# Kernel tuning notes

Hardware: AMD Instinct MI355X
Metric: run time of the kernel (lower is better)

## Reference

```python
import jax, jax.numpy as jnp
import numpy as np

A = 3                      # anchors per location
HS = [256, 128, 64, 32]    # square feature-map sizes (FPN levels)
B = 4                      # batch (num images)
SIZES = [A * h * h for h in HS]
T = sum(SIZES)             # 261120 anchors per image
PRE_N, POST_N = 512, 512
NMS_TH, SCORE_TH, MIN_SIZE = 0.7, 0.0, 1e-3
LOG_MAX = 4.135166556742356   # log(1000/16), standard delta clamp
MAXV = 8                      # max vertices of quad-quad intersection
LVL_OFF = 8192.0              # per-level coordinate offset for batched NMS


def box_corners(b):
    # b: [..., 5] (cx, cy, w, h, angle) -> [..., 4, 2] CCW corners
    cx, cy, w, h, a = (b[..., i] for i in range(5))
    c, s = jnp.cos(a), jnp.sin(a)
    dx = 0.5 * jnp.stack([w, -w, -w, w], -1)
    dy = 0.5 * jnp.stack([h, h, -h, -h], -1)
    x = cx[..., None] + dx * c[..., None] - dy * s[..., None]
    y = cy[..., None] + dx * s[..., None] + dy * c[..., None]
    return jnp.stack([x, y], -1)


def _clip(poly, cnt, p1, p2):
    # Sutherland-Hodgman clip of poly (padded [MAXV,2], cnt valid) by half-plane left of p1->p2
    e = p2 - p1
    d = e[0] * (poly[:, 1] - p1[1]) - e[1] * (poly[:, 0] - p1[0])
    def body(carry, i):
        out, oc = carry
        nxt = jnp.where(i + 1 < cnt, i + 1, 0)
        cur_in, nxt_in = d[i] >= 0, d[nxt] >= 0
        valid = i < cnt
        keep = valid & cur_in
        out = out.at[oc].set(jnp.where(keep, poly[i], out[oc]))
        oc = oc + keep.astype(jnp.int32)
        crs = valid & (cur_in != nxt_in)
        den = d[i] - d[nxt]
        t = d[i] / jnp.where(den == 0, 1.0, den)
        ip = poly[i] + t * (poly[nxt] - poly[i])
        out = out.at[oc].set(jnp.where(crs, ip, out[oc]))
        oc = oc + crs.astype(jnp.int32)
        return (out, oc), None
    (out, oc), _ = jax.lax.scan(body, (jnp.zeros((MAXV, 2), poly.dtype), jnp.int32(0)), jnp.arange(MAXV))
    return out, oc


def _inter_area(ca, cb):
    # intersection area of two convex quads given CCW corners [4,2]
    poly = jnp.zeros((MAXV, 2), ca.dtype).at[:4].set(ca)
    cnt = jnp.int32(4)
    for k in range(4):
        poly, cnt = _clip(poly, cnt, cb[k], cb[(k + 1) % 4])
    i = jnp.arange(MAXV)
    nxt = jnp.where(i + 1 < cnt, i + 1, 0)
    cr = poly[i, 0] * poly[nxt, 1] - poly[nxt, 0] * poly[i, 1]
    area = 0.5 * jnp.abs(jnp.sum(jnp.where(i < cnt, cr, 0.0)))
    return jnp.where(cnt >= 3, area, 0.0)


def decode(deltas, anchors):
    # XYWHA decode with 6-dim deltas (dx,dy,dw,dh,dsin,dcos), weights all 1.0
    ax, ay, aw, ah, aa = (anchors[..., i] for i in range(5))
    dx, dy, dw, dh, ds, dc = (deltas[..., i] for i in range(6))
    dw = jnp.minimum(dw, LOG_MAX)
    dh = jnp.minimum(dh, LOG_MAX)
    return jnp.stack([ax + dx * aw, ay + dy * ah, aw * jnp.exp(dw),
                      ah * jnp.exp(dh), aa + jnp.arctan2(ds, dc)], -1)


def nms_image(boxes, scores, levels):
    # boxes [N,5], scores [N] (post-sigmoid), levels [N] int32 -> fixed-size padded outputs
    N = scores.shape[0]
    valid = (boxes[:, 2] >= MIN_SIZE) & (boxes[:, 3] >= MIN_SIZE) & (scores >= SCORE_TH)
    s = jnp.where(valid, scores, -jnp.inf)
    order = jnp.argsort(-s)
    bx, sc, vd = boxes[order], s[order], valid[order]
    off = levels[order].astype(bx.dtype) * LVL_OFF
    nb = bx.at[:, :2].add(off[:, None])          # level offset => cross-level IoU == 0
    nbg = jax.lax.stop_gradient(nb)
    corners = box_corners(nbg)                    # [N,4,2]
    areas = nbg[:, 2] * nbg[:, 3]
    CH = 128
    def chunk_fn(args):
        cc, ca = args
        def row(ci, ai):
            inter = jax.vmap(lambda cj: _inter_area(ci, cj))(corners)
            return inter / (ai + areas - inter + 1e-7)
        return jax.vmap(row)(cc, ca)
    iou = jax.lax.map(chunk_fn, (corners.reshape(N // CH, CH, 4, 2),
                                 areas.reshape(N // CH, CH))).reshape(N, N)
    idx = jnp.arange(N)
    def body(i, sup):
        keep_i = ~sup[i]
        return sup | (keep_i & (iou[i] > NMS_TH) & (idx > i))
    sup = jax.lax.fori_loop(0, N, body, ~vd)      # invalid boxes start suppressed
    kept = ~sup
    _, top_i = jax.lax.top_k(jnp.where(kept, sc, -jnp.inf), POST_N)
    ok = kept[top_i]
    return jnp.where(ok[:, None], bx[top_i], 0.0), jnp.where(ok, sc[top_i], 0.0)


def rpn_forward(objs, dlts, anchors):
    obj_f, dlt_f = [], []
    for o, d, h in zip(objs, dlts, HS):
        # permute_and_flatten: [B,A,H,W] -> [B,H*W*A]; [B,A*6,H,W] -> [B,H*W*A,6]
        obj_f.append(o.transpose(0, 2, 3, 1).reshape(B, -1))
        dlt_f.append(d.reshape(B, A, 6, h, h).transpose(0, 3, 4, 1, 2).reshape(B, -1, 6))
    objectness = jnp.concatenate(obj_f, 1)        # [B, T]
    deltas = jnp.concatenate(dlt_f, 1)            # [B, T, 6]
    proposals = decode(deltas, anchors)           # [B, T, 5]
    parts, offset = [], 0
    for sz in SIZES:                               # per-level top-k
        k = min(PRE_N, sz)
        _, ti = jax.lax.top_k(objectness[:, offset:offset + sz], k)
        parts.append(ti + offset)
        offset += sz
    top_idx = jnp.concatenate(parts, 1)           # [B, 4*PRE_N]
    levels = jnp.concatenate([jnp.full((sz,), i, jnp.int32) for i, sz in enumerate(SIZES)])
    obj_top = jnp.take_along_axis(objectness, top_idx, 1)
    prop_top = jnp.take_along_axis(proposals, top_idx[..., None], 1)
    lvl_top = levels[top_idx]
    scores = jax.nn.sigmoid(obj_top)
    return jax.vmap(nms_image)(prop_top, scores, lvl_top)


def setup_inputs() -> dict:
    key = jax.random.key(0)
    ks = jax.random.split(key, 9)
    inp = {}
    for i, h in enumerate(HS):
        inp[f"obj{i}"] = jax.random.normal(ks[i], (B, A, h, h), jnp.float32)
        inp[f"dlt{i}"] = 0.25 * jax.random.normal(ks[4 + i], (B, A * 6, h, h), jnp.float32)
    u = jax.random.uniform(ks[8], (B, T, 5), jnp.float32)
    inp["anchors"] = jnp.stack([u[..., 0] * 1024.0, u[..., 1] * 1024.0,
                                8.0 + 120.0 * u[..., 2], 8.0 + 120.0 * u[..., 3],
                                jnp.pi * (u[..., 4] - 0.5)], -1)
    return inp


def reference(obj0, obj1, obj2, obj3, dlt0, dlt1, dlt2, dlt3, anchors):
    # returns (boxes [B, POST_N, 5], scores [B, POST_N]) padded with zeros
    return rpn_forward([obj0, obj1, obj2, obj3], [dlt0, dlt1, dlt2, dlt3], anchors)
```

## Files before the change

### kernel.cpp

```cpp
#include <hip/hip_runtime.h>

typedef unsigned int u32;
typedef unsigned long long u64;
typedef unsigned char u8;

#define NB 4
#define T_ANCH 261120
#define NCAND 2048
#define KSEL 512
#define POSTN 512
#define LOG_MAXF 4.135166556742356f
#define NMS_TH 0.7f
#define LVL_OFF_F 8192.0f
#define BINS 4096
#define EQCAP 8192
#define K4A_BLOCKS 2048
#define K4A_ROWS 4
#define K1_BLOCKS 256

__device__ __forceinline__ u32 mono32(float f){
  u32 u = __float_as_uint(f);
  return (u & 0x80000000u) ? ~u : (u | 0x80000000u);
}
__device__ __forceinline__ int lvl_hw(int lvl){ return 65536 >> (2*lvl); }
__device__ __forceinline__ int lvl_off(int lvl){
  return (lvl>0?196608:0) + (lvl>1?49152:0) + (lvl>2?12288:0);
}
__device__ __forceinline__ void k1_map(int bx, int& b, int& lvl, int& ch){
  b = bx >> 6;
  int c = bx & 63;
  if (c < 48){ lvl = 0; ch = c; }
  else if (c < 60){ lvl = 1; ch = c - 48; }
  else if (c < 63){ lvl = 2; ch = c - 60; }
  else { lvl = 3; ch = 0; }
}

__global__ __launch_bounds__(1024) void k1_hist_thresh(
    const float* __restrict__ o0, const float* __restrict__ o1,
    const float* __restrict__ o2, const float* __restrict__ o3,
    u32* __restrict__ hist16, u32* __restrict__ done16,
    u32* __restrict__ gb0, u32* __restrict__ gcA)
{
  int b, lvl, ch;
  k1_map(blockIdx.x, b, lvl, ch);
  int bid16 = b*4 + lvl;
  int nch = (lvl==0?48 : lvl==1?12 : lvl==2?3 : 1);
  const float* ob = (lvl==0)?o0 : (lvl==1)?o1 : (lvl==2)?o2 : o3;
  int hw = lvl_hw(lvl);
  int size = 3*hw;
  int n4 = size >> 2;
  int i4 = ch*1024 + threadIdx.x;
  __shared__ u32 hist[BINS];
  __shared__ u32 coarse[64];
  __shared__ int s_last;
  for (int i = threadIdx.x; i < BINS; i += 1024) hist[i] = 0;
  __syncthreads();
  if (i4 < n4){
    float4 v = ((const float4*)(ob + (size_t)b*size))[i4];
    atomicAdd(&hist[mono32(v.x) >> 20], 1u);
    atomicAdd(&hist[mono32(v.y) >> 20], 1u);
    atomicAdd(&hist[mono32(v.z) >> 20], 1u);
    atomicAdd(&hist[mono32(v.w) >> 20], 1u);
  }
  __syncthreads();
  u32* gh = hist16 + (size_t)bid16*BINS;
  for (int i = threadIdx.x; i < BINS; i += 1024){
    u32 c = hist[i];
    if (c) atomicAdd(&gh[i], c);
  }
  __syncthreads();
  if (threadIdx.x == 0){
    __threadfence();
    u32 d = atomicAdd(&done16[bid16], 1u);
    s_last = (d == (u32)(nch - 1)) ? 1 : 0;
  }
  __syncthreads();
  if (!s_last) return;

  __threadfence();
  for (int i = threadIdx.x; i < BINS; i += 1024)
    hist[i] = __hip_atomic_load(&gh[i], __ATOMIC_RELAXED, __HIP_MEMORY_SCOPE_AGENT);
  __syncthreads();
  int t = threadIdx.x;
  if (t < 64){
    u32 s = 0;
    for (int z = 0; z < 64; ++z) s += hist[t*64 + z];
    coarse[t] = s;
  }
  __syncthreads();
  if (t == 0){
    u32 acc = 0;
    int cb = 63;
    while (acc + coarse[cb] < (u32)KSEL){ acc += coarse[cb]; --cb; }
    int z = cb*64 + 63;
    while (acc + hist[z] < (u32)KSEL){ acc += hist[z]; --z; }
    gb0[bid16] = (u32)z;
    gcA[bid16] = acc;
  }
}

__global__ __launch_bounds__(1024) void k2_classify(
    const float* __restrict__ o0, const float* __restrict__ o1,
    const float* __restrict__ o2, const float* __restrict__ o3,
    const u32* __restrict__ gb0,
    u32* __restrict__ emitcnt, u32* __restrict__ tiecnt,
    int* __restrict__ cand_j, u64* __restrict__ gtie)
{
  int b, lvl, ch;
  k1_map(blockIdx.x, b, lvl, ch);
  int bid16 = b*4 + lvl;
  const float* ob = (lvl==0)?o0 : (lvl==1)?o1 : (lvl==2)?o2 : o3;
  int hw = lvl_hw(lvl);
  int size = 3*hw;
  int n4 = size >> 2;
  int i4 = ch*1024 + threadIdx.x;

  __shared__ u32 dbuf[KSEL];
  __shared__ u64 tbuf[4096];
  __shared__ u32 dn, tn, dbase, tbase;
  if (threadIdx.x == 0){ dn = 0; tn = 0; }
  __syncthreads();

  u32 b0v = gb0[bid16];
  if (i4 < n4){
    float4 v = ((const float4*)(ob + (size_t)b*size))[i4];
    int L = i4 << 2;
    int a = L / hw;
    int pix = L - a*hw;
    int j0 = pix*3 + a;
    float vv[4] = {v.x, v.y, v.z, v.w};
    #pragma unroll
    for (int q = 0; q < 4; ++q){
      u32 m = mono32(vv[q]);
      u32 bin = m >> 20;
      int j = j0 + 3*q;
      if (bin > b0v){
        u32 s = atomicAdd(&dn, 1u);
        if (s < (u32)KSEL) dbuf[s] = (u32)j;
      } else if (bin == b0v){
        u32 s = atomicAdd(&tn, 1u);
        if (s < 4096u) tbuf[s] = ((u64)m << 32) | (u32)(~(u32)j);
      }
    }
  }
  __syncthreads();
  if (threadIdx.x == 0){
    dbase = dn ? atomicAdd(&emitcnt[bid16], dn) : 0u;
    tbase = tn ? atomicAdd(&tiecnt[bid16], tn) : 0u;
  }
  __syncthreads();
  for (u32 x = threadIdx.x; x < dn; x += 1024){
    u32 s = dbase + x;
    if (s < (u32)KSEL) cand_j[bid16*KSEL + s] = (int)dbuf[x];
  }
  for (u32 x = threadIdx.x; x < tn; x += 1024){
    u32 s = tbase + x;
    if (s < (u32)EQCAP) gtie[(size_t)bid16*EQCAP + s] = tbuf[x];
  }
}

__global__ __launch_bounds__(512) void k3_tie_decode(
    const u64* __restrict__ gtie, const u32* __restrict__ tiecnt,
    const u32* __restrict__ gcA, const int* __restrict__ cand_j,
    const float* __restrict__ o0, const float* __restrict__ o1,
    const float* __restrict__ o2, const float* __restrict__ o3,
    const float* __restrict__ d0, const float* __restrict__ d1,
    const float* __restrict__ d2, const float* __restrict__ d3,
    const float* __restrict__ anchors,
    float* __restrict__ cscore, u32* __restrict__ csmono,
    u64* __restrict__ ctb, float* __restrict__ cbox, u8* __restrict__ cvalid)
{
  int bid = blockIdx.x;
  int t = threadIdx.x;
  __shared__ u64 eq[EQCAP];
  __shared__ u32 wbuf[KSEL];
  __shared__ int jlist[KSEL];
  __shared__ u32 wn;
  u32 n = tiecnt[bid]; if (n > (u32)EQCAP) n = (u32)EQCAP;
  u32 cA = gcA[bid];
  u32 k = (u32)KSEL - cA;
  if (t == 0) wn = 0;
  for (int i = t; i < KSEL; i += 512) jlist[i] = 0;
  for (u32 i = t; i < n; i += 512) eq[i] = gtie[(size_t)bid*EQCAP + i];
  __syncthreads();
  for (u32 i = t; i < n; i += 512){
    u64 ki = eq[i];
    u32 r = 0;
    for (u32 m = 0; m < n; ++m) r += (eq[m] > ki) ? 1u : 0u;
    if (r < k){
      u32 s = atomicAdd(&wn, 1u);
      if (s < (u32)KSEL) wbuf[s] = (u32)(~(u32)ki);
    }
  }
  __syncthreads();
  u32 w = wn;
  for (u32 i = t; i < cA; i += 512)
    if (i < (u32)KSEL) jlist[i] = cand_j[bid*KSEL + i];
  for (u32 x = t; x < w; x += 512){
    u32 s = cA + x;
    if (s < (u32)KSEL) jlist[s] = (int)wbuf[x];
  }
  __syncthreads();

  {
    int c = bid*KSEL + t;
    int b = bid >> 2, lvl = bid & 3;
    int j = jlist[t];
    int hw = lvl_hw(lvl);
    u32 pix = (u32)j / 3u;
    u32 a = (u32)j - pix*3u;
    const float* ob = (lvl==0)?o0 : (lvl==1)?o1 : (lvl==2)?o2 : o3;
    const float* dl = (lvl==0)?d0 : (lvl==1)?d1 : (lvl==2)?d2 : d3;

    float ov = ob[(size_t)(b*3 + (int)a)*hw + pix];
    size_t dbase = ((size_t)(b*3 + (int)a)*6)*(size_t)hw + pix;
    float dx  = dl[dbase + 0*(size_t)hw];
    float dy  = dl[dbase + 1*(size_t)hw];
    float dw  = dl[dbase + 2*(size_t)hw];
    float dh  = dl[dbase + 3*(size_t)hw];
    float dsn = dl[dbase + 4*(size_t)hw];
    float dcs = dl[dbase + 5*(size_t)hw];
    int tt = lvl_off(lvl) + j;
    const float* an = anchors + ((size_t)b*T_ANCH + tt)*5;
    float ax=an[0], ay=an[1], aw=an[2], ah=an[3], aa=an[4];
    dw = fminf(dw, LOG_MAXF); dh = fminf(dh, LOG_MAXF);
    float cx = ax + dx*aw;
    float cy = ay + dy*ah;
    float ww = aw * expf(dw);
    float hh = ah * expf(dh);
    float ang = aa + atan2f(dsn, dcs);
    double sd = 1.0 / (1.0 + exp(-(double)ov));
    float sc = (float)sd;
    bool valid = (ww >= 1e-3f) && (hh >= 1e-3f) && (sc >= 0.0f);
    cscore[c] = sc;
    csmono[c] = valid ? mono32(sc) : 0u;
    ctb[c] = ((u64)lvl << 50) | ((u64)(u32)(~mono32(ov)) << 18) | (u64)(u32)j;
    cvalid[c] = valid ? 1 : 0;
    float* bb = cbox + (size_t)c*5;
    bb[0]=cx; bb[1]=cy; bb[2]=ww; bb[3]=hh; bb[4]=ang;
  }
}

__global__ __launch_bounds__(256) void k4_rank(
    const u32* __restrict__ csmono, const u64* __restrict__ ctb,
    const float* __restrict__ cscore, const float* __restrict__ cbox,
    const u8* __restrict__ cvalid,
    float* __restrict__ sscore, float* __restrict__ sbox,
    float* __restrict__ geom, float4* __restrict__ aabb4,
    u8* __restrict__ svalid)
{
  int b   = blockIdx.x >> 6;
  int blk = blockIdx.x & 63;
  __shared__ u32 sm[NCAND];
  __shared__ u64 stb[NCAND];
  __shared__ u32 cnt[32][8];
  for (int k = threadIdx.x; k < NCAND; k += 256){
    sm[k]  = csmono[b*NCAND + k];
    stb[k] = ctb[b*NCAND + k];
  }
  __syncthreads();
  int esub = threadIdx.x >> 3;
  int ssub = threadIdx.x & 7;
  int id = blk*32 + esub;
  u32 ms = sm[id];
  u64 mt = stb[id];
  u32 r = 0;
  #pragma unroll 8
  for (int it = 0; it < 256; ++it){
    int m = it*8 + ssub;
    u32 s2 = sm[m]; u64 t2 = stb[m];
    r += ((s2 > ms) || (s2 == ms && t2 < mt)) ? 1u : 0u;
  }
  cnt[esub][ssub] = r;
  __syncthreads();
  if (ssub == 0){
    u32 rank = 0;
    #pragma unroll
    for (int q = 0; q < 8; ++q) rank += cnt[esub][q];
    int gsrc = b*NCAND + id;
    int gdst = b*NCAND + (int)rank;
    sscore[gdst] = cscore[gsrc];
    svalid[gdst] = cvalid[gsrc];
    float b0 = cbox[(size_t)gsrc*5+0], b1 = cbox[(size_t)gsrc*5+1];
    float b2 = cbox[(size_t)gsrc*5+2], b3 = cbox[(size_t)gsrc*5+3];
    float b4 = cbox[(size_t)gsrc*5+4];
    float* sb = sbox + (size_t)gdst*5;
    sb[0]=b0; sb[1]=b1; sb[2]=b2; sb[3]=b3; sb[4]=b4;
    int lvl = (int)((mt >> 50) & 3ull);
    float offv = (float)lvl * LVL_OFF_F;
    float cx = b0 + offv, cy = b1 + offv, w=b2, h=b3, ang=b4;
    float cc = cosf(ang), sn = sinf(ang);
    float hx = 0.5f*w, hy = 0.5f*h;
    float x0 = cx + hx*cc - hy*sn, y0 = cy + hx*sn + hy*cc;
    float x1 = cx - hx*cc - hy*sn, y1 = cy - hx*sn + hy*cc;
    float x2 = cx - hx*cc + hy*sn, y2 = cy - hx*sn - hy*cc;
    float x3 = cx + hx*cc + hy*sn, y3 = cy + hx*sn - hy*cc;
    float minx = fminf(fminf(x0,x1),fminf(x2,x3));
    float maxx = fmaxf(fmaxf(x0,x1),fmaxf(x2,x3));
    float miny = fminf(fminf(y0,y1),fminf(y2,y3));
    float maxy = fmaxf(fmaxf(y0,y1),fmaxf(y2,y3));
    float* g = geom + (size_t)gdst*16;
    g[0]=minx; g[1]=maxx; g[2]=miny; g[3]=maxy; g[4]=w*h;
    g[5]=x0; g[6]=y0; g[7]=x1; g[8]=y1; g[9]=x2; g[10]=y2; g[11]=x3; g[12]=y3;
    aabb4[gdst] = make_float4(minx, maxx, miny, maxy);
  }
}

__device__ __forceinline__ void emit_pt(float* ox, float* oy, int oc, float x, float y){
  #pragma unroll
  for (int s = 0; s < 8; ++s) if (s == oc){ ox[s] = x; oy[s] = y; }
}

__device__ float quad_inter(const float* ca, const float* cb){
  float px[8], py[8];
  #pragma unroll
  for (int q = 0; q < 8; ++q){ px[q]=0.f; py[q]=0.f; }
  #pragma unroll
  for (int q = 0; q < 4; ++q){ px[q]=ca[2*q]; py[q]=ca[2*q+1]; }
  int cnt = 4;
  #pragma unroll
  for (int e = 0; e < 4; ++e){
    float p1x = cb[2*e],         p1y = cb[2*e+1];
    float p2x = cb[(2*e+2)&7],   p2y = cb[(2*e+3)&7];
    float ex = p2x-p1x, ey = p2y-p1y;
    float d[8];
    #pragma unroll
    for (int q = 0; q < 8; ++q) d[q] = ex*(py[q]-p1y) - ey*(px[q]-p1x);
    float ox[8], oy[8];
    #pragma unroll
    for (int q = 0; q < 8; ++q){ ox[q]=0.f; oy[q]=0.f; }
    int oc = 0;
    #pragma unroll
    for (int q = 0; q < 8; ++q){
      if (q < cnt){
        bool last = (q+1 >= cnt);
        float dn  = last ? d[0]  : d[(q+1)&7];
        bool in0 = (d[q] >= 0.0f), in1 = (dn >= 0.0f);
        if (in0){ emit_pt(ox,oy,oc,px[q],py[q]); oc++; }
        if (in0 != in1){
          float pnx = last ? px[0] : px[(q+1)&7];
          float pny = last ? py[0] : py[(q+1)&7];
          float den = d[q] - dn;
          float t = d[q] / ((den == 0.0f) ? 1.0f : den);
          emit_pt(ox,oy,oc, px[q] + t*(pnx-px[q]), py[q] + t*(pny-py[q]));
          oc++;
        }
      }
    }
    cnt = (oc > 8) ? 8 : oc;
    #pragma unroll
    for (int q = 0; q < 8; ++q){ px[q]=ox[q]; py[q]=oy[q]; }
  }
  if (cnt < 3) return 0.0f;
  float s = 0.0f;
  #pragma unroll
  for (int q = 0; q < 8; ++q){
    if (q < cnt){
      bool last = (q+1 >= cnt);
      float pnx = last ? px[0] : px[(q+1)&7];
      float pny = last ? py[0] : py[(q+1)&7];
      s += px[q]*pny - pnx*py[q];
    }
  }
  return 0.5f*fabsf(s);
}

__global__ __launch_bounds__(256) void k5_pairs(
    const float4* __restrict__ aabb4, const float* __restrict__ geom,
    u64* __restrict__ mask, u64* __restrict__ rowflag)
{
  __shared__ u32 lbuf[K4A_ROWS*NCAND];
  __shared__ u32 lcnt;
  if (threadIdx.x == 0) lcnt = 0;
  __syncthreads();
  int img = blockIdx.x >> 9;
  int i0  = (blockIdx.x & 511) * K4A_ROWS;
  #pragma unroll
  for (int r = 0; r < K4A_ROWS; ++r){
    int i = i0 + r;
    float4 gi = aabb4[img*NCAND + i];
    for (int j = threadIdx.x; j < NCAND; j += 256){
      bool pass = false;
      if (j > i){
        float4 gj = aabb4[img*NCAND + j];
        pass = !(gi.x > gj.y || gj.x > gi.y || gi.z > gj.w || gj.z > gi.w);
      }
      if (pass){
        u32 s = atomicAdd(&lcnt, 1u);
        lbuf[s] = (u32)((i << 11) | j);
      }
    }
  }
  __syncthreads();
  u32 n = lcnt;
  for (u32 x = threadIdx.x; x < n; x += 256){
    u32 gt = lbuf[x];
    int i = (int)(gt >> 11);
    int j = (int)(gt & (NCAND-1));
    const float* gi = geom + ((size_t)(img*NCAND + i))*16;
    const float* gj = geom + ((size_t)(img*NCAND + j))*16;
    float inter = quad_inter(gi+5, gj+5);
    float iou = inter / (gi[4] + gj[4] - inter + 1e-7f);
    if (iou > NMS_TH){
      atomicOr(&mask[((size_t)(img*NCAND + i))*32 + (j >> 6)], 1ull << (j & 63));
      atomicOr(&rowflag[(size_t)img*32 + (i >> 6)], 1ull << (i & 63));
    }
  }
}

__global__ __launch_bounds__(1024) void k6_nms_out(
    const u64* __restrict__ mask, const u64* __restrict__ rowflag,
    const u8* __restrict__ svalid,
    const float* __restrict__ sbox, const float* __restrict__ sscore,
    float* __restrict__ out)
{
  int b = blockIdx.x;
  __shared__ u32 fid[NCAND];
  __shared__ u32 wcnt[32], wpref[32];
  __shared__ u64 s_kept[32];
  __shared__ u32 pref[32];
  __shared__ u32 s_F;
  int t = threadIdx.x;
  int wid = t >> 6, lane = t & 63;

  if (t < 32) wcnt[t] = (u32)__popcll(rowflag[b*32 + t]);
  __syncthreads();
  if (t == 0){
    u32 run = 0;
    for (int w = 0; w < 32; ++w){ wpref[w] = run; run += wcnt[w]; }
    s_F = run;
  }
  __syncthreads();
  if (t < 32){
    u64 fw = rowflag[b*32 + t];
    u32 o = wpref[t];
    while (fw){
      int bpos = __builtin_ctzll(fw);
      fid[o++] = (u32)(t*64 + bpos);
      fw &= fw - 1;
    }
  }
  for (int x = t; x < POSTN*5; x += 1024) out[(size_t)b*POSTN*5 + x] = 0.0f;
  for (int x = t; x < POSTN;   x += 1024) out[(size_t)NB*POSTN*5 + b*POSTN + x] = 0.0f;
  __syncthreads();

  if (wid == 0){
    u32 slo = 0, shi = 0;
    {
      int wl = lane & 31;
      u64 w = 0;
      for (int q = 0; q < 64; ++q)
        if (!svalid[b*NCAND + wl*64 + q]) w |= (1ull << q);
      slo = (u32)w; shi = (u32)(w >> 32);
    }
    u32 F = s_F;
    const u64* mb = mask + ((size_t)b*NCAND)*32;
    for (u32 f = 0; f < F; f += 8){
      u32 myfid = 0;
      if (f + (lane & 7) < F) myfid = fid[f + (lane & 7)];
      u64 v[8];
      #pragma unroll
      for (int q = 0; q < 8; ++q){
        if (f + q < F){
          u32 fq = (u32)__builtin_amdgcn_readlane((int)myfid, q);
          v[q] = mb[(size_t)fq*32 + (lane & 31)];
        } else v[q] = 0ull;
      }
      #pragma unroll
      for (int q = 0; q < 8; ++q){
        if (f + q < F){
          u32 i = (u32)__builtin_amdgcn_readlane((int)myfid, q);
          int wi = (int)(i >> 6);
          u32 wlo = (u32)__builtin_amdgcn_readlane((int)slo, wi);
          u32 whi = (u32)__builtin_amdgcn_readlane((int)shi, wi);
          u64 w = ((u64)whi << 32) | wlo;
          u32 keep = (u32)((~w >> (i & 63)) & 1ull);
          u64 vm = v[q] & (0ull - (u64)keep);
          slo |= (u32)vm; shi |= (u32)(vm >> 32);
        }
      }
    }
    if (lane < 32) s_kept[lane] = ~(((u64)shi << 32) | slo);
  }
  __syncthreads();

  if (t < 32) pref[t] = (u32)__popcll(s_kept[t]);
  __syncthreads();
  if (t == 0){
    u32 run = 0;
    for (int w = 0; w < 32; ++w){ u32 tv = pref[w]; pref[w] = run; run += tv; }
  }
  __syncthreads();
  for (int i = t; i < NCAND; i += 1024){
    u64 kw = s_kept[i >> 6];
    if ((kw >> (i & 63)) & 1ull){
      u32 rank = pref[i >> 6] + (u32)__popcll(kw & ((1ull << (i & 63)) - 1ull));
      if (rank < POSTN){
        const float* bp = sbox + ((size_t)(b*NCAND + i))*5;
        float* op = out + ((size_t)(b*POSTN + rank))*5;
        op[0]=bp[0]; op[1]=bp[1]; op[2]=bp[2]; op[3]=bp[3]; op[4]=bp[4];
        out[(size_t)NB*POSTN*5 + b*POSTN + rank] = sscore[b*NCAND + i];
      }
    }
  }
}

extern "C" void kernel_launch(void* const* d_in, const int* in_sizes, int n_in,
                              void* d_out, int out_size, void* d_ws, size_t ws_size,
                              hipStream_t stream)
{
  (void)out_size; (void)ws_size;
  const float *obj[4] = {nullptr,nullptr,nullptr,nullptr};
  const float *dlt[4] = {nullptr,nullptr,nullptr,nullptr};
  const float *anchors = nullptr;
  for (int i = 0; i < n_in; ++i){
    int s = in_sizes[i];
    const float* p = (const float*)d_in[i];
    switch (s){
      case 786432:  obj[0] = p; break;
      case 4718592: dlt[0] = p; break;
      case 196608:  obj[1] = p; break;
      case 1179648: dlt[1] = p; break;
      case 49152:   obj[2] = p; break;
      case 294912:  dlt[2] = p; break;
      case 12288:   obj[3] = p; break;
      case 73728:   dlt[3] = p; break;
      case 5222400: anchors = p; break;
      default: break;
    }
  }

  char* wsb = (char*)d_ws;
  size_t off = 0;
  auto alloc = [&](size_t bytes)->void*{
    size_t cur = (off + 255) & ~(size_t)255;
    off = cur + bytes;
    return (void*)(wsb + cur);
  };
  int*   cand_j = (int*)  alloc(16*KSEL*sizeof(int));
  float* cscore = (float*)alloc((size_t)NB*NCAND*sizeof(float));
  u32*   csmono = (u32*)  alloc((size_t)NB*NCAND*sizeof(u32));
  u64*   ctb    = (u64*)  alloc((size_t)NB*NCAND*sizeof(u64));
  float* cbox   = (float*)alloc((size_t)NB*NCAND*5*sizeof(float));
  u8*    cvalid = (u8*)   alloc((size_t)NB*NCAND);
  float* sscore = (float*)alloc((size_t)NB*NCAND*sizeof(float));
  float* sbox   = (float*)alloc((size_t)NB*NCAND*5*sizeof(float));
  u8*    svalid = (u8*)   alloc((size_t)NB*NCAND);
  float* geom   = (float*)alloc((size_t)NB*NCAND*16*sizeof(float));
  float4* aabb4 = (float4*)alloc((size_t)NB*NCAND*sizeof(float4));
  u64*   gtie   = (u64*)  alloc((size_t)16*EQCAP*sizeof(u64));
  u32*   gb0    = (u32*)  alloc(16*sizeof(u32));
  u32*   gcA    = (u32*)  alloc(16*sizeof(u32));
  size_t mask_bytes = (size_t)NB*NCAND*32*sizeof(u64);
  u64*   maskp  = (u64*)  alloc(mask_bytes);
  u64*   rowflag= (u64*)  alloc((size_t)NB*32*sizeof(u64));
  u32*   hist16 = (u32*)  alloc((size_t)16*BINS*sizeof(u32));
  u32*   done16 = (u32*)  alloc(16*sizeof(u32));
  u32*   emitc  = (u32*)  alloc(16*sizeof(u32));
  u32*   tiec   = (u32*)  alloc(16*sizeof(u32));
  size_t zero_len = (size_t)((wsb + off) - (char*)maskp);

  hipMemsetAsync(maskp, 0, zero_len, stream);

  hipLaunchKernelGGL(k1_hist_thresh, dim3(K1_BLOCKS), dim3(1024), 0, stream,
                     obj[0], obj[1], obj[2], obj[3], hist16, done16, gb0, gcA);
  hipLaunchKernelGGL(k2_classify, dim3(K1_BLOCKS), dim3(1024), 0, stream,
                     obj[0], obj[1], obj[2], obj[3], gb0, emitc, tiec,
                     cand_j, gtie);
  hipLaunchKernelGGL(k3_tie_decode, dim3(16), dim3(512), 0, stream,
                     gtie, tiec, gcA, cand_j,
                     obj[0], obj[1], obj[2], obj[3],
                     dlt[0], dlt[1], dlt[2], dlt[3],
                     anchors, cscore, csmono, ctb, cbox, cvalid);
  hipLaunchKernelGGL(k4_rank, dim3(256), dim3(256), 0, stream,
                     csmono, ctb, cscore, cbox, cvalid, sscore, sbox, geom,
                     aabb4, svalid);
  hipLaunchKernelGGL(k5_pairs, dim3(K4A_BLOCKS), dim3(256), 0, stream,
                     aabb4, geom, maskp, rowflag);
  hipLaunchKernelGGL(k6_nms_out, dim3(4), dim3(1024), 0, stream,
                     maskp, rowflag, svalid, sbox, sscore, (float*)d_out);
}
```

Baseline: 204.6 us.

## Balance NMS pair rows, ballot-aggregate atomics, move mask zeroing into rank kernel

The pair-test kernel now gives each block two low rows and two mirrored high rows, so the triangular j>i work per block is roughly equal. The inner loop starts at i+1, and wave-level ballot plus a single atomicAdd per wave compacts the passing pairs, replacing one shared atomic per pair. The 2 MB mask and rowflag zeroing moves out of the memset and into the rank kernel, so the memset covers only the small counters. The local buffer shrinks to 4096 entries, which still holds the worst case for the balanced rows (about 4096 pairs).

New measurement: 192.3 us. 6.0% less time.

```diff
diff --git a/kernel.cpp b/kernel.cpp
--- a/kernel.cpp
+++ b/kernel.cpp
@@ -14,8 +14,7 @@
 #define LVL_OFF_F 8192.0f
 #define BINS 4096
 #define EQCAP 8192
-#define K4A_BLOCKS 2048
-#define K4A_ROWS 4
+#define K5_BLOCKS 2048
 #define K1_BLOCKS 256
 
 __device__ __forceinline__ u32 mono32(float f){
@@ -247,13 +246,18 @@
     const u8* __restrict__ cvalid,
     float* __restrict__ sscore, float* __restrict__ sbox,
     float* __restrict__ geom, float4* __restrict__ aabb4,
-    u8* __restrict__ svalid)
+    u8* __restrict__ svalid, u64* __restrict__ maskz, u64* __restrict__ rowflagz)
 {
   int b   = blockIdx.x >> 6;
   int blk = blockIdx.x & 63;
   __shared__ u32 sm[NCAND];
   __shared__ u64 stb[NCAND];
   __shared__ u32 cnt[32][8];
+  {
+    u64* mz = maskz + (size_t)blockIdx.x * 1024;
+    for (int x = threadIdx.x; x < 1024; x += 256) mz[x] = 0ull;
+    if (threadIdx.x == 0 && blockIdx.x < NB*32) rowflagz[blockIdx.x] = 0ull;
+  }
   for (int k = threadIdx.x; k < NCAND; k += 256){
     sm[k]  = csmono[b*NCAND + k];
     stb[k] = ctb[b*NCAND + k];
@@ -369,25 +373,31 @@
     const float4* __restrict__ aabb4, const float* __restrict__ geom,
     u64* __restrict__ mask, u64* __restrict__ rowflag)
 {
-  __shared__ u32 lbuf[K4A_ROWS*NCAND];
+  __shared__ u32 lbuf[4096];
   __shared__ u32 lcnt;
   if (threadIdx.x == 0) lcnt = 0;
   __syncthreads();
   int img = blockIdx.x >> 9;
-  int i0  = (blockIdx.x & 511) * K4A_ROWS;
+  int kk  = blockIdx.x & 511;
+  int lane = threadIdx.x & 63;
+  int rows[4] = {2*kk, 2*kk + 1, 2046 - 2*kk, 2047 - 2*kk};
   #pragma unroll
-  for (int r = 0; r < K4A_ROWS; ++r){
-    int i = i0 + r;
+  for (int r = 0; r < 4; ++r){
+    int i = rows[r];
     float4 gi = aabb4[img*NCAND + i];
-    for (int j = threadIdx.x; j < NCAND; j += 256){
-      bool pass = false;
-      if (j > i){
-        float4 gj = aabb4[img*NCAND + j];
-        pass = !(gi.x > gj.y || gj.x > gi.y || gi.z > gj.w || gj.z > gi.w);
-      }
-      if (pass){
-        u32 s = atomicAdd(&lcnt, 1u);
-        lbuf[s] = (u32)((i << 11) | j);
+    for (int j = i + 1 + (int)threadIdx.x; j < NCAND; j += 256){
+      float4 gj = aabb4[img*NCAND + j];
+      bool pass = !(gi.x > gj.y || gj.x > gi.y || gi.z > gj.w || gj.z > gi.w);
+      u64 bm = __ballot(pass);
+      if (bm){
+        int leader = __ffsll((long long)bm) - 1;
+        u32 base = 0;
+        if (lane == leader) base = atomicAdd(&lcnt, (u32)__popcll(bm));
+        base = (u32)__shfl((int)base, leader);
+        if (pass){
+          u32 off = (u32)__popcll(bm & ((1ull << lane) - 1ull));
+          lbuf[base + off] = (u32)((i << 11) | j);
+        }
       }
     }
   }
@@ -549,18 +559,17 @@
   float* geom   = (float*)alloc((size_t)NB*NCAND*16*sizeof(float));
   float4* aabb4 = (float4*)alloc((size_t)NB*NCAND*sizeof(float4));
   u64*   gtie   = (u64*)  alloc((size_t)16*EQCAP*sizeof(u64));
+  u64*   maskp  = (u64*)  alloc((size_t)NB*NCAND*32*sizeof(u64));
+  u64*   rowflag= (u64*)  alloc((size_t)NB*32*sizeof(u64));
   u32*   gb0    = (u32*)  alloc(16*sizeof(u32));
   u32*   gcA    = (u32*)  alloc(16*sizeof(u32));
-  size_t mask_bytes = (size_t)NB*NCAND*32*sizeof(u64);
-  u64*   maskp  = (u64*)  alloc(mask_bytes);
-  u64*   rowflag= (u64*)  alloc((size_t)NB*32*sizeof(u64));
   u32*   hist16 = (u32*)  alloc((size_t)16*BINS*sizeof(u32));
   u32*   done16 = (u32*)  alloc(16*sizeof(u32));
   u32*   emitc  = (u32*)  alloc(16*sizeof(u32));
   u32*   tiec   = (u32*)  alloc(16*sizeof(u32));
-  size_t zero_len = (size_t)((wsb + off) - (char*)maskp);
-
-  hipMemsetAsync(maskp, 0, zero_len, stream);
+  size_t zero_len = (size_t)((wsb + off) - (char*)hist16);
+
+  hipMemsetAsync(hist16, 0, zero_len, stream);
 
   hipLaunchKernelGGL(k1_hist_thresh, dim3(K1_BLOCKS), dim3(1024), 0, stream,
                      obj[0], obj[1], obj[2], obj[3], hist16, done16, gb0, gcA);
@@ -574,8 +583,8 @@
                      anchors, cscore, csmono, ctb, cbox, cvalid);
   hipLaunchKernelGGL(k4_rank, dim3(256), dim3(256), 0, stream,
                      csmono, ctb, cscore, cbox, cvalid, sscore, sbox, geom,
-                     aabb4, svalid);
-  hipLaunchKernelGGL(k5_pairs, dim3(K4A_BLOCKS), dim3(256), 0, stream,
+                     aabb4, svalid, maskp, rowflag);
+  hipLaunchKernelGGL(k5_pairs, dim3(K5_BLOCKS), dim3(256), 0, stream,
                      aabb4, geom, maskp, rowflag);
   hipLaunchKernelGGL(k6_nms_out, dim3(4), dim3(1024), 0, stream,
                      maskp, rowflag, svalid, sbox, sscore, (float*)d_out);
```
